# Kernel tuning notes

Measured on AMD Instinct MI355X. Metric: run time of the kernel, lower is better.

Reference implementation:

```python
import jax, jax.numpy as jnp
import numpy as np

N, K, D = 524288, 64, 2
EPS = 1e-6
LOG_2PI = float(np.log(2.0 * np.pi))


def setup_inputs() -> dict:
    key = jax.random.key(0)
    k1, k2, k3, k4 = jax.random.split(key, 4)
    x = jax.random.normal(k1, (N, D), dtype=jnp.float32) * 2.0
    means = jax.random.normal(k2, (K, D), dtype=jnp.float32)
    # cholesky factor param: identity plus small noise (tril applied in forward)
    chol_var = jnp.eye(D, dtype=jnp.float32)[None] + 0.1 * jax.random.normal(k3, (K, D, D), dtype=jnp.float32)
    pi = jax.random.uniform(k4, (K,), dtype=jnp.float32)
    return {"x": x, "means": means, "chol_var": chol_var, "pi": pi}


def reference(x, means, chol_var, pi):
    # x: [N, D]; means: [K, D]; chol_var: [K, D, D]; pi: [K]
    K_, D_ = means.shape
    L = jnp.tril(chol_var)                                   # [K, D, D]
    cov = L @ jnp.swapaxes(L, -1, -2) + EPS * jnp.eye(D_, dtype=x.dtype)
    chol = jnp.linalg.cholesky(cov)                          # [K, D, D] lower
    logdet = 2.0 * jnp.sum(jnp.log(jnp.diagonal(chol, axis1=-2, axis2=-1)), axis=-1)  # [K]
    cinv = jnp.linalg.inv(chol)                              # [K, D, D] (tiny DxD)
    diff = x[:, None, :] - means[None, :, :]                 # [N, K, D]
    y = jnp.einsum('kij,nkj->nki', cinv, diff)               # whitened residuals
    quad = jnp.sum(y * y, axis=-1)                           # [N, K] Mahalanobis^2
    log_probs = -0.5 * (D_ * LOG_2PI + logdet[None, :] + quad)  # [N, K]
    weighted = log_probs + jax.nn.log_softmax(pi)            # [N, K]
    return jax.nn.logsumexp(weighted, axis=1)                # [N]
```

## Files before the change

### kernel.cpp

```cpp
#include <hip/hip_runtime.h>
#include <hip/hip_bf16.h>
#include <math.h>
#include <stdint.h>

#define LOG_2PI_D 1.837877066409345483560659472811
#define LOG2E_D   1.442695040888963407359924681002
#define LN2_F     0.69314718055994530942f

typedef float v2f __attribute__((ext_vector_type(2)));

__device__ __forceinline__ float rl(float v, int l) {
    return __builtin_bit_cast(float,
        __builtin_amdgcn_readlane(__builtin_bit_cast(int, v), l));
}

__global__ __launch_bounds__(256, 2) void gmm_fused(
        const float* __restrict__ x,
        const float* __restrict__ means,
        const float* __restrict__ chol_var,
        const float* __restrict__ pi,
        float* __restrict__ out,
        int n2) {
    const int lane = threadIdx.x & 63;

    {
    }
    const int k = lane;
    float p = pi[k];
    float mx = p;
    #pragma unroll
    for (int off = 32; off > 0; off >>= 1) mx = fmaxf(mx, __shfl_xor(mx, off, 64));
    float sf = __expf(p - mx);
    #pragma unroll
    for (int off = 32; off > 0; off >>= 1) sf += __shfl_xor(sf, off, 64);
    double logpi = (double)p - (double)mx - (double)__logf(sf);

    double v00 = (double)chol_var[k*4 + 0];
    double v10 = (double)chol_var[k*4 + 2];
    double v11 = (double)chol_var[k*4 + 3];
    const double eps = 1e-6;
    double cov00 = v00*v00 + eps;
    double cov01 = v00*v10;
    double cov11 = v10*v10 + v11*v11 + eps;
    double a  = sqrt(cov00);
    double b  = cov01 / a;
    double c2 = cov11 - b*b;
    double logdet = (double)__logf((float)(cov00 * c2));
    double P00 = 1.0/cov00 + (b*b)/(cov00*c2);
    double P01 = -b/(a*c2);
    double P11 = 1.0/c2;
    double m0 = (double)means[k*2 + 0];
    double m1 = (double)means[k*2 + 1];
    double constk = -0.5*(2.0*LOG_2PI_D + logdet) + logpi;

    float C0 = (float)(-0.5*P00*LOG2E_D);
    float C1 = (float)(-P01*LOG2E_D);
    float C2 = (float)(-0.5*P11*LOG2E_D);
    float C3 = (float)((P00*m0 + P01*m1)*LOG2E_D);
    float C4 = (float)((P01*m0 + P11*m1)*LOG2E_D);
    float C5 = (float)((constk
                 - 0.5*(P00*m0*m0 + 2.0*P01*m0*m1 + P11*m1*m1))*LOG2E_D);

    int i = blockIdx.x * 256 + threadIdx.x;
    if (i >= n2) return;

    float4 xv = reinterpret_cast<const float4*>(x)[i];
    v2f X0  = { xv.x, xv.z };
    v2f X1  = { xv.y, xv.w };
    v2f Q00 = X0 * X0;
    v2f Q01 = X0 * X1;
    v2f Q11 = X1 * X1;

    v2f w2[64];
    v2f m2 = { -INFINITY, -INFINITY };
    #pragma unroll
    for (int kk = 0; kk < 64; ++kk) {
        float c0 = rl(C0, kk), c1 = rl(C1, kk), c2f = rl(C2, kk);
        float c3 = rl(C3, kk), c4 = rl(C4, kk), c5 = rl(C5, kk);
        v2f t = { c5, c5 };
        t = __builtin_elementwise_fma((v2f){c0, c0}, Q00, t);
        t = __builtin_elementwise_fma((v2f){c1, c1}, Q01, t);
        t = __builtin_elementwise_fma((v2f){c2f, c2f}, Q11, t);
        t = __builtin_elementwise_fma((v2f){c3, c3}, X0,  t);
        t = __builtin_elementwise_fma((v2f){c4, c4}, X1,  t);
        w2[kk] = t;
        m2 = __builtin_elementwise_max(m2, t);
    }

    float sa0 = 0.f, sa1 = 0.f, sb0 = 0.f, sb1 = 0.f;
    #pragma unroll
    for (int kk = 0; kk < 64; kk += 2) {
        v2f d0 = w2[kk]     - m2;
        v2f d1 = w2[kk + 1] - m2;
        sa0 += __builtin_amdgcn_exp2f(d0.x);
        sb0 += __builtin_amdgcn_exp2f(d0.y);
        sa1 += __builtin_amdgcn_exp2f(d1.x);
        sb1 += __builtin_amdgcn_exp2f(d1.y);
    }
    float2 o;
    o.x = LN2_F * (m2.x + __builtin_amdgcn_logf(sa0 + sa1));
    o.y = LN2_F * (m2.y + __builtin_amdgcn_logf(sb0 + sb1));
    reinterpret_cast<float2*>(out)[i] = o;
}

extern "C" void kernel_launch(void* const* d_in, const int* in_sizes, int n_in,
                              void* d_out, int out_size, void* d_ws, size_t ws_size,
                              hipStream_t stream) {
    const float* x        = (const float*)d_in[0];
    const float* means    = (const float*)d_in[1];
    const float* chol_var = (const float*)d_in[2];
    const float* pi       = (const float*)d_in[3];
    float* out = (float*)d_out;

    int n  = in_sizes[0] / 2;
    int n2 = n / 2;
    int blocks = (n2 + 255) / 256;

    gmm_fused<<<blocks, 256, 0, stream>>>(x, means, chol_var, pi, out, n2);
}
```

Baseline: 71.40 us.

## Split per-component coefficient setup into separate kernel read via scalar constant loads

```diff
diff --git a/kernel.cpp b/kernel.cpp
--- a/kernel.cpp
+++ b/kernel.cpp
@@ -8,24 +8,14 @@
 #define LN2_F     0.69314718055994530942f
 
 typedef float v2f __attribute__((ext_vector_type(2)));
+typedef const float __attribute__((address_space(4))) cfloat;
 
-__device__ __forceinline__ float rl(float v, int l) {
-    return __builtin_bit_cast(float,
-        __builtin_amdgcn_readlane(__builtin_bit_cast(int, v), l));
-}
+__global__ void gmm_setup(const float* __restrict__ means,
+                          const float* __restrict__ chol_var,
+                          const float* __restrict__ pi,
+                          float* __restrict__ coef) {
+    int k = threadIdx.x;
 
-__global__ __launch_bounds__(256, 2) void gmm_fused(
-        const float* __restrict__ x,
-        const float* __restrict__ means,
-        const float* __restrict__ chol_var,
-        const float* __restrict__ pi,
-        float* __restrict__ out,
-        int n2) {
-    const int lane = threadIdx.x & 63;
-
-    {
-    }
-    const int k = lane;
     float p = pi[k];
     float mx = p;
     #pragma unroll
@@ -53,16 +43,23 @@
     double m1 = (double)means[k*2 + 1];
     double constk = -0.5*(2.0*LOG_2PI_D + logdet) + logpi;
 
-    float C0 = (float)(-0.5*P00*LOG2E_D);
-    float C1 = (float)(-P01*LOG2E_D);
-    float C2 = (float)(-0.5*P11*LOG2E_D);
-    float C3 = (float)((P00*m0 + P01*m1)*LOG2E_D);
-    float C4 = (float)((P01*m0 + P11*m1)*LOG2E_D);
-    float C5 = (float)((constk
-                 - 0.5*(P00*m0*m0 + 2.0*P01*m0*m1 + P11*m1*m1))*LOG2E_D);
+    coef[k*6 + 0] = (float)(-0.5*P00*LOG2E_D);
+    coef[k*6 + 1] = (float)(-P01*LOG2E_D);
+    coef[k*6 + 2] = (float)(-0.5*P11*LOG2E_D);
+    coef[k*6 + 3] = (float)((P00*m0 + P01*m1)*LOG2E_D);
+    coef[k*6 + 4] = (float)((P01*m0 + P11*m1)*LOG2E_D);
+    coef[k*6 + 5] = (float)((constk
+                     - 0.5*(P00*m0*m0 + 2.0*P01*m0*m1 + P11*m1*m1))*LOG2E_D);
+}
 
+__global__ __launch_bounds__(256, 2) void gmm_main(const float* __restrict__ x,
+                                                   const float* __restrict__ coef,
+                                                   float* __restrict__ out,
+                                                   int n2) {
     int i = blockIdx.x * 256 + threadIdx.x;
     if (i >= n2) return;
+
+    cfloat* cc = (cfloat*)(uintptr_t)coef;
 
     float4 xv = reinterpret_cast<const float4*>(x)[i];
     v2f X0  = { xv.x, xv.z };
@@ -74,24 +71,23 @@
     v2f w2[64];
     v2f m2 = { -INFINITY, -INFINITY };
     #pragma unroll
-    for (int kk = 0; kk < 64; ++kk) {
-        float c0 = rl(C0, kk), c1 = rl(C1, kk), c2f = rl(C2, kk);
-        float c3 = rl(C3, kk), c4 = rl(C4, kk), c5 = rl(C5, kk);
-        v2f t = { c5, c5 };
-        t = __builtin_elementwise_fma((v2f){c0, c0}, Q00, t);
+    for (int k = 0; k < 64; ++k) {
+        float c0 = cc[k*6+0], c1 = cc[k*6+1], c2 = cc[k*6+2];
+        float c3 = cc[k*6+3], c4 = cc[k*6+4], c5 = cc[k*6+5];
+        v2f t = __builtin_elementwise_fma((v2f){c0, c0}, Q00, (v2f){c5, c5});
         t = __builtin_elementwise_fma((v2f){c1, c1}, Q01, t);
-        t = __builtin_elementwise_fma((v2f){c2f, c2f}, Q11, t);
+        t = __builtin_elementwise_fma((v2f){c2, c2}, Q11, t);
         t = __builtin_elementwise_fma((v2f){c3, c3}, X0,  t);
         t = __builtin_elementwise_fma((v2f){c4, c4}, X1,  t);
-        w2[kk] = t;
+        w2[k] = t;
         m2 = __builtin_elementwise_max(m2, t);
     }
 
     float sa0 = 0.f, sa1 = 0.f, sb0 = 0.f, sb1 = 0.f;
     #pragma unroll
-    for (int kk = 0; kk < 64; kk += 2) {
-        v2f d0 = w2[kk]     - m2;
-        v2f d1 = w2[kk + 1] - m2;
+    for (int k = 0; k < 64; k += 2) {
+        v2f d0 = w2[k]     - m2;
+        v2f d1 = w2[k + 1] - m2;
         sa0 += __builtin_amdgcn_exp2f(d0.x);
         sb0 += __builtin_amdgcn_exp2f(d0.y);
         sa1 += __builtin_amdgcn_exp2f(d1.x);
@@ -110,11 +106,13 @@
     const float* means    = (const float*)d_in[1];
     const float* chol_var = (const float*)d_in[2];
     const float* pi       = (const float*)d_in[3];
-    float* out = (float*)d_out;
+    float* out  = (float*)d_out;
+    float* coef = (float*)d_ws;
 
     int n  = in_sizes[0] / 2;
     int n2 = n / 2;
     int blocks = (n2 + 255) / 256;
 
-    gmm_fused<<<blocks, 256, 0, stream>>>(x, means, chol_var, pi, out, n2);
+    gmm_setup<<<1, 64, 0, stream>>>(means, chol_var, pi, coef);
+    gmm_main<<<blocks, 256, 0, stream>>>(x, coef, out, n2);
 }
```

New measurement: 70.20 us. No clear change (-1.7%).
